# Performance work log

Hardware: AMD Instinct MI355X
Metric: run time of the kernel (lower is better)

The kernel has to match this reference:

```python
import jax, jax.numpy as jnp
import numpy as np

NUM_TYPES = 4
IN_DIM = 128
HID_DIM = 256
OUT_DIM = 128
NUM_NODES = 100000


def setup_inputs() -> dict:
    key = jax.random.key(0)
    k_x, k_t, k_w1, k_b1, k_w2, k_b2 = jax.random.split(key, 6)
    raw_features = jax.random.normal(k_x, (NUM_NODES, IN_DIM), dtype=jnp.float32)
    node_type = jax.random.randint(k_t, (NUM_NODES,), 0, NUM_TYPES, dtype=jnp.int64)
    # stacked per-type MLP params (Kaiming-ish scale like torch Linear defaults)
    W1 = jax.random.uniform(k_w1, (NUM_TYPES, IN_DIM, HID_DIM), dtype=jnp.float32,
                            minval=-1.0, maxval=1.0) / np.sqrt(IN_DIM)
    b1 = jax.random.uniform(k_b1, (NUM_TYPES, HID_DIM), dtype=jnp.float32,
                            minval=-1.0, maxval=1.0) / np.sqrt(IN_DIM)
    W2 = jax.random.uniform(k_w2, (NUM_TYPES, HID_DIM, OUT_DIM), dtype=jnp.float32,
                            minval=-1.0, maxval=1.0) / np.sqrt(HID_DIM)
    b2 = jax.random.uniform(k_b2, (NUM_TYPES, OUT_DIM), dtype=jnp.float32,
                            minval=-1.0, maxval=1.0) / np.sqrt(HID_DIM)
    return {"raw_features": raw_features, "node_type": node_type,
            "W1": W1, "b1": b1, "W2": W2, "b2": b2}


def reference(raw_features, node_type, W1, b1, W2, b2):
    # Run every expert on every node (num_types is tiny), then select per node.
    # h: [types, nodes, hidden]
    h = jax.nn.relu(jnp.einsum('ni,tih->tnh', raw_features, W1) + b1[:, None, :])
    # out_all: [types, nodes, out]
    out_all = jnp.einsum('tnh,tho->tno', h, W2) + b2[:, None, :]
    # select expert output matching each node's type -> [nodes, out]
    encoded = out_all[node_type, jnp.arange(raw_features.shape[0])]
    return encoded
```

## Files before the change

kernel.cpp:

```cpp
#include <hip/hip_runtime.h>
#include <hip/hip_bf16.h>

typedef float f32x4 __attribute__((ext_vector_type(4)));
typedef short short8 __attribute__((ext_vector_type(8)));

#define NTYPES 4


static __device__ __forceinline__ unsigned short f2bf(float f) {
  union { float f; unsigned int u; } v; v.f = f;
  unsigned int u = v.u;
  unsigned int r = u + 0x7FFFu + ((u >> 16) & 1u);
  return (unsigned short)(r >> 16);
}

static __device__ __forceinline__ unsigned int pkbf(float a, float b) {
  __hip_bfloat162 h = __float22bfloat162_rn(make_float2(a, b));
  union { __hip_bfloat162 h; unsigned int u; } v; v.h = h;
  return v.u;
}

__global__ __launch_bounds__(256) void k_prep(const float* __restrict__ W1,
                                              const float* __restrict__ W2,
                                              unsigned short* __restrict__ W1T,
                                              unsigned short* __restrict__ W2T,
                                              int* __restrict__ meta) {
  __shared__ unsigned short s[64][72];
  const int tid = threadIdx.x;
  const int b = blockIdx.x;
  if (b == 0 && tid < 16) meta[tid] = 0;
  const int bb = b & 31;
  const int t = bb >> 3, ti = bb & 7;
  const float* src; unsigned short* dst; int scols, tr, tc;
  if (b < 32) { src = W1 + t * 32768; dst = W1T + t * 32768; scols = 256; tr = ti >> 2; tc = ti & 3; }
  else        { src = W2 + t * 32768; dst = W2T + t * 32768; scols = 128; tr = ti >> 1; tc = ti & 1; }
  const int srows = 32768 / scols;
  const int r0 = tid >> 4, c4 = (tid & 15) << 2;
  #pragma unroll
  for (int i = 0; i < 4; ++i) {
    int r = tr * 64 + i * 16 + r0;
    float4 v = *(const float4*)(src + r * scols + tc * 64 + c4);
    s[i * 16 + r0][c4 + 0] = f2bf(v.x);
    s[i * 16 + r0][c4 + 1] = f2bf(v.y);
    s[i * 16 + r0][c4 + 2] = f2bf(v.z);
    s[i * 16 + r0][c4 + 3] = f2bf(v.w);
  }
  __syncthreads();
  #pragma unroll
  for (int i = 0; i < 4; ++i) {
    int orow = i * 16 + r0;
    ushort4 u;
    u.x = s[c4 + 0][orow];
    u.y = s[c4 + 1][orow];
    u.z = s[c4 + 2][orow];
    u.w = s[c4 + 3][orow];
    *(ushort4*)(dst + (tc * 64 + orow) * srows + tr * 64 + c4) = u;
  }
}

__global__ __launch_bounds__(256) void k_hist(const int* __restrict__ NT, int n,
                                              int* __restrict__ meta) {
  __shared__ int c[NTYPES];
  if (threadIdx.x < NTYPES) c[threadIdx.x] = 0;
  __syncthreads();
  int i = blockIdx.x * 256 + threadIdx.x;
  if (i < n) atomicAdd(&c[NT[i]], 1);
  __syncthreads();
  if (threadIdx.x < NTYPES && c[threadIdx.x] > 0)
    atomicAdd(&meta[threadIdx.x], c[threadIdx.x]);
}

__global__ __launch_bounds__(256) void k_scatter(const int* __restrict__ NT, int n,
                                                 int* __restrict__ meta,
                                                 int* __restrict__ perm) {
  __shared__ int cnt[NTYPES];
  __shared__ int cbase[NTYPES];
  __shared__ int sb[NTYPES + 1];
  if (threadIdx.x < NTYPES) cnt[threadIdx.x] = 0;
  if (threadIdx.x == 0) {
    int b = 0; sb[0] = 0;
    for (int t = 0; t < NTYPES; ++t) {
      b += (meta[t] + 63) & ~63;
      sb[t + 1] = b;
    }
  }
  __syncthreads();
  int i = blockIdx.x * 256 + threadIdx.x;
  int t = 0, r = 0;
  bool valid = (i < n);
  if (valid) { t = NT[i]; r = atomicAdd(&cnt[t], 1); }
  __syncthreads();
  if (threadIdx.x < NTYPES)
    cbase[threadIdx.x] = atomicAdd(&meta[4 + threadIdx.x], cnt[threadIdx.x]);
  __syncthreads();
  if (valid) perm[sb[t] + cbase[t] + r] = i;
  if (blockIdx.x == 0) {
    if (threadIdx.x <= NTYPES) meta[8 + threadIdx.x] = sb[threadIdx.x];
    int tt = threadIdx.x >> 6, j = threadIdx.x & 63;
    int p = sb[tt] + meta[tt] + j;
    if (p < sb[tt + 1]) perm[p] = -1;
  }
}

__global__ __launch_bounds__(256, 1) void k_mlpw(
    const float* __restrict__ X, const int* __restrict__ perm,
    const int* __restrict__ meta,
    const unsigned short* __restrict__ W1T, const unsigned short* __restrict__ W2T,
    const float* __restrict__ B1, const float* __restrict__ B2,
    float* __restrict__ OUT, float* __restrict__ dump) {
  __shared__ __align__(16) unsigned char x_lds[16384];
  __shared__ __align__(16) unsigned char h_lds[32768];
  __shared__ int s_rid[2][64];

  const int tid = threadIdx.x;
  const int l  = tid & 63, w = tid >> 6;
  const int lo = l & 15,  hi = l >> 4;
  const int rg = tid >> 5;
  const int c4 = (tid & 31) * 4;

  const int t  = blockIdx.x >> 7;
  const int lb = blockIdx.x & 127;
  const int g0 = meta[8 + t] >> 6;
  const int g1 = meta[9 + t] >> 6;
  const int nt = g1 - g0 - lb;
  if (nt <= 0) return;
  const int cnt = (nt + 127) >> 7;

  if (tid < 64) s_rid[0][tid] = perm[(g0 + lb) * 64 + tid];
  __syncthreads();
  float4 xv[8];
  #pragma unroll
  for (int p = 0; p < 8; ++p) {
    int row = p * 8 + rg;
    int rd = s_rid[0][row];
    xv[p] = make_float4(0.f, 0.f, 0.f, 0.f);
    if (rd >= 0) xv[p] = *(const float4*)(X + (size_t)rd * 128 + c4);
  }

  const unsigned short* w1t = W1T + (t << 15);
  const unsigned short* w2t = W2T + (t << 15);
  short8 a1[4][4];
  #pragma unroll
  for (int ks = 0; ks < 4; ++ks)
    #pragma unroll
    for (int m = 0; m < 4; ++m)
      a1[ks][m] = *(const short8*)(w1t + (w * 64 + m * 16 + lo) * 128 + ks * 32 + hi * 8);
  short8 a2[8][2];
  #pragma unroll
  for (int ks = 0; ks < 8; ++ks)
    #pragma unroll
    for (int mo = 0; mo < 2; ++mo)
      a2[ks][mo] = *(const short8*)(w2t + (w * 32 + mo * 16 + lo) * 256 + ks * 32 + hi * 8);
  f32x4 bb1[4], bb2[2];
  #pragma unroll
  for (int m = 0; m < 4; ++m)
    bb1[m] = *(const f32x4*)(B1 + t * 256 + w * 64 + m * 16 + hi * 4);
  #pragma unroll
  for (int mo = 0; mo < 2; ++mo)
    bb2[mo] = *(const f32x4*)(B2 + t * 128 + w * 32 + mo * 16 + hi * 4);

  for (int j = 0; j < cnt; ++j) {
    const int g = g0 + lb + j * 128;
    const bool hn = (j + 1 < cnt);
    const int cur = j & 1, nxt = cur ^ 1;

    #pragma unroll
    for (int p = 0; p < 8; ++p) {
      int row = p * 8 + rg;
      uint2 u;
      u.x = pkbf(xv[p].x, xv[p].y);
      u.y = pkbf(xv[p].z, xv[p].w);
      int byte = (row * 256 + c4 * 2) ^ ((row & 7) << 4);
      *(uint2*)(x_lds + byte) = u;
    }
    __syncthreads();

    if (hn && tid < 64) s_rid[nxt][tid] = perm[(g + 128) * 64 + tid];

    f32x4 acc[4][4];
    #pragma unroll
    for (int m = 0; m < 4; ++m)
      #pragma unroll
      for (int n = 0; n < 4; ++n) acc[m][n] = (f32x4){0.f, 0.f, 0.f, 0.f};
    #pragma unroll
    for (int ks = 0; ks < 4; ++ks) {
      short8 b[4];
      #pragma unroll
      for (int n = 0; n < 4; ++n) {
        int row = n * 16 + lo;
        int byte = (row * 256 + ks * 64 + hi * 16) ^ ((row & 7) << 4);
        b[n] = *(const short8*)(x_lds + byte);
      }
      #pragma unroll
      for (int m = 0; m < 4; ++m)
        #pragma unroll
        for (int n = 0; n < 4; ++n)
          acc[m][n] = __builtin_amdgcn_mfma_f32_16x16x32_bf16(a1[ks][m], b[n], acc[m][n], 0, 0, 0);
    }

    #pragma unroll
    for (int m = 0; m < 4; ++m) {
      const int hw2 = w * 128 + m * 32 + hi * 8;
      #pragma unroll
      for (int n = 0; n < 4; ++n) {
        int node = n * 16 + lo;
        uint2 hu;
        hu.x = pkbf(fmaxf(acc[m][n][0] + bb1[m][0], 0.f),
                    fmaxf(acc[m][n][1] + bb1[m][1], 0.f));
        hu.y = pkbf(fmaxf(acc[m][n][2] + bb1[m][2], 0.f),
                    fmaxf(acc[m][n][3] + bb1[m][3], 0.f));
        int byte = (node * 512 + hw2) ^ ((node & 7) << 4);
        *(uint2*)(h_lds + byte) = hu;
      }
    }
    __syncthreads();

    float4 nv[8];
    #pragma unroll
    for (int p = 0; p < 8; ++p) nv[p] = make_float4(0.f, 0.f, 0.f, 0.f);
    if (hn) {
      #pragma unroll
      for (int p = 0; p < 8; ++p) {
        int rd = s_rid[nxt][p * 8 + rg];
        if (rd >= 0) nv[p] = *(const float4*)(X + (size_t)rd * 128 + c4);
      }
    }

    f32x4 acc2[2][4];
    #pragma unroll
    for (int mo = 0; mo < 2; ++mo)
      #pragma unroll
      for (int n = 0; n < 4; ++n) acc2[mo][n] = (f32x4){0.f, 0.f, 0.f, 0.f};
    #pragma unroll
    for (int ks = 0; ks < 8; ++ks) {
      short8 b[4];
      #pragma unroll
      for (int n = 0; n < 4; ++n) {
        int node = n * 16 + lo;
        int byte = (node * 512 + ks * 64 + hi * 16) ^ ((node & 7) << 4);
        b[n] = *(const short8*)(h_lds + byte);
      }
      #pragma unroll
      for (int mo = 0; mo < 2; ++mo)
        #pragma unroll
        for (int n = 0; n < 4; ++n)
          acc2[mo][n] = __builtin_amdgcn_mfma_f32_16x16x32_bf16(a2[ks][mo], b[n], acc2[mo][n], 0, 0, 0);
    }
    __syncthreads();

    #pragma unroll
    for (int mo = 0; mo < 2; ++mo) {
      const int oc = w * 32 + mo * 16 + hi * 4;
      #pragma unroll
      for (int n = 0; n < 4; ++n) {
        int node = n * 16 + lo;
        f32x4 o = acc2[mo][n];
        o[0] += bb2[mo][0]; o[1] += bb2[mo][1];
        o[2] += bb2[mo][2]; o[3] += bb2[mo][3];
        int byte = (node * 512 + oc * 4) ^ ((node & 7) << 4);
        *(f32x4*)(h_lds + byte) = o;
      }
    }
    __syncthreads();

    #pragma unroll
    for (int p = 0; p < 8; ++p) {
      int row = p * 8 + rg;
      int rd = s_rid[cur][row];
      f32x4 v = *(const f32x4*)(h_lds + ((row * 512 + c4 * 4) ^ ((row & 7) << 4)));
      float* dst = (rd >= 0) ? (OUT + (size_t)rd * 128 + c4) : (dump + c4);
      *(f32x4*)dst = v;
    }

    #pragma unroll
    for (int p = 0; p < 8; ++p) xv[p] = nv[p];
  }
}

extern "C" void kernel_launch(void* const* d_in, const int* in_sizes, int n_in,
                              void* d_out, int out_size, void* d_ws, size_t ws_size,
                              hipStream_t stream) {
  const float* X  = (const float*)d_in[0];
  const int*   NT = (const int*)d_in[1];
  const float* W1 = (const float*)d_in[2];
  const float* B1 = (const float*)d_in[3];
  const float* W2 = (const float*)d_in[4];
  const float* B2 = (const float*)d_in[5];
  float* OUT = (float*)d_out;
  const int n = in_sizes[1];

  char* ws = (char*)d_ws;
  int* meta = (int*)ws;
  float* dump = (float*)(ws + 512);
  int* perm = (int*)(ws + 1024);
  unsigned short* W1T = (unsigned short*)(ws + 402432);
  unsigned short* W2T = (unsigned short*)(ws + 664576);

  k_prep<<<64, 256, 0, stream>>>(W1, W2, W1T, W2T, meta);
  const int nb = (n + 255) / 256;
  k_hist<<<nb, 256, 0, stream>>>(NT, n, meta);
  k_scatter<<<nb, 256, 0, stream>>>(NT, n, meta, perm);
  k_mlpw<<<512, 256, 0, stream>>>(X, perm, meta, W1T, W2T, B1, B2, OUT, dump);
}
```

Baseline: 58.45 us.

## Fuse prep, histogram, scatter and MLP into one cooperative kernel

Replaces the four-kernel pipeline (weight transpose, histogram, scatter, grouped MLP) with a single cooperative kernel of 256 blocks that uses grid-wide syncs between phases. The histogram becomes per-block counts with a deterministic prefix sum instead of global atomics, which also removes the meta zeroing dependency. This removes three kernel launch gaps. In exchange the MLP phase runs with only 256 blocks (64 per type) rather than 512, and two grid barriers are added. A three-kernel fallback path runs if the cooperative launch fails.

```diff
diff --git a/kernel.cpp b/kernel.cpp
--- a/kernel.cpp
+++ b/kernel.cpp
@@ -1,10 +1,14 @@
 #include <hip/hip_runtime.h>
 #include <hip/hip_bf16.h>
+#include <hip/hip_cooperative_groups.h>
+
+namespace cg = cooperative_groups;
 
 typedef float f32x4 __attribute__((ext_vector_type(4)));
 typedef short short8 __attribute__((ext_vector_type(8)));
 
 #define NTYPES 4
+#define GRIDC 256
 
 
 static __device__ __forceinline__ unsigned short f2bf(float f) {
@@ -20,119 +24,61 @@
   return v.u;
 }
 
-__global__ __launch_bounds__(256) void k_prep(const float* __restrict__ W1,
-                                              const float* __restrict__ W2,
-                                              unsigned short* __restrict__ W1T,
-                                              unsigned short* __restrict__ W2T,
-                                              int* __restrict__ meta) {
-  __shared__ unsigned short s[64][72];
-  const int tid = threadIdx.x;
-  const int b = blockIdx.x;
-  if (b == 0 && tid < 16) meta[tid] = 0;
-  const int bb = b & 31;
-  const int t = bb >> 3, ti = bb & 7;
+static __device__ __forceinline__ void prep_tile(int role, int tid,
+    const float* __restrict__ W1, const float* __restrict__ W2,
+    unsigned short* __restrict__ W1T, unsigned short* __restrict__ W2T,
+    unsigned short (*sp)[72]) {
+  const int bb = role & 31;
+  const int tt = bb >> 3, ti = bb & 7;
   const float* src; unsigned short* dst; int scols, tr, tc;
-  if (b < 32) { src = W1 + t * 32768; dst = W1T + t * 32768; scols = 256; tr = ti >> 2; tc = ti & 3; }
-  else        { src = W2 + t * 32768; dst = W2T + t * 32768; scols = 128; tr = ti >> 1; tc = ti & 1; }
+  if (role < 32) { src = W1 + tt * 32768; dst = W1T + tt * 32768; scols = 256; tr = ti >> 2; tc = ti & 3; }
+  else           { src = W2 + tt * 32768; dst = W2T + tt * 32768; scols = 128; tr = ti >> 1; tc = ti & 1; }
   const int srows = 32768 / scols;
-  const int r0 = tid >> 4, c4 = (tid & 15) << 2;
+  const int r0 = tid >> 4, cw = (tid & 15) << 2;
   #pragma unroll
   for (int i = 0; i < 4; ++i) {
     int r = tr * 64 + i * 16 + r0;
-    float4 v = *(const float4*)(src + r * scols + tc * 64 + c4);
-    s[i * 16 + r0][c4 + 0] = f2bf(v.x);
-    s[i * 16 + r0][c4 + 1] = f2bf(v.y);
-    s[i * 16 + r0][c4 + 2] = f2bf(v.z);
-    s[i * 16 + r0][c4 + 3] = f2bf(v.w);
+    float4 v = *(const float4*)(src + r * scols + tc * 64 + cw);
+    sp[i * 16 + r0][cw + 0] = f2bf(v.x);
+    sp[i * 16 + r0][cw + 1] = f2bf(v.y);
+    sp[i * 16 + r0][cw + 2] = f2bf(v.z);
+    sp[i * 16 + r0][cw + 3] = f2bf(v.w);
   }
   __syncthreads();
   #pragma unroll
   for (int i = 0; i < 4; ++i) {
     int orow = i * 16 + r0;
     ushort4 u;
-    u.x = s[c4 + 0][orow];
-    u.y = s[c4 + 1][orow];
-    u.z = s[c4 + 2][orow];
-    u.w = s[c4 + 3][orow];
-    *(ushort4*)(dst + (tc * 64 + orow) * srows + tr * 64 + c4) = u;
-  }
-}
-
-__global__ __launch_bounds__(256) void k_hist(const int* __restrict__ NT, int n,
-                                              int* __restrict__ meta) {
-  __shared__ int c[NTYPES];
-  if (threadIdx.x < NTYPES) c[threadIdx.x] = 0;
-  __syncthreads();
-  int i = blockIdx.x * 256 + threadIdx.x;
-  if (i < n) atomicAdd(&c[NT[i]], 1);
-  __syncthreads();
-  if (threadIdx.x < NTYPES && c[threadIdx.x] > 0)
-    atomicAdd(&meta[threadIdx.x], c[threadIdx.x]);
-}
-
-__global__ __launch_bounds__(256) void k_scatter(const int* __restrict__ NT, int n,
-                                                 int* __restrict__ meta,
-                                                 int* __restrict__ perm) {
-  __shared__ int cnt[NTYPES];
-  __shared__ int cbase[NTYPES];
-  __shared__ int sb[NTYPES + 1];
-  if (threadIdx.x < NTYPES) cnt[threadIdx.x] = 0;
-  if (threadIdx.x == 0) {
-    int b = 0; sb[0] = 0;
-    for (int t = 0; t < NTYPES; ++t) {
-      b += (meta[t] + 63) & ~63;
-      sb[t + 1] = b;
-    }
-  }
-  __syncthreads();
-  int i = blockIdx.x * 256 + threadIdx.x;
-  int t = 0, r = 0;
-  bool valid = (i < n);
-  if (valid) { t = NT[i]; r = atomicAdd(&cnt[t], 1); }
-  __syncthreads();
-  if (threadIdx.x < NTYPES)
-    cbase[threadIdx.x] = atomicAdd(&meta[4 + threadIdx.x], cnt[threadIdx.x]);
-  __syncthreads();
-  if (valid) perm[sb[t] + cbase[t] + r] = i;
-  if (blockIdx.x == 0) {
-    if (threadIdx.x <= NTYPES) meta[8 + threadIdx.x] = sb[threadIdx.x];
-    int tt = threadIdx.x >> 6, j = threadIdx.x & 63;
-    int p = sb[tt] + meta[tt] + j;
-    if (p < sb[tt + 1]) perm[p] = -1;
-  }
-}
-
-__global__ __launch_bounds__(256, 1) void k_mlpw(
+    u.x = sp[cw + 0][orow];
+    u.y = sp[cw + 1][orow];
+    u.z = sp[cw + 2][orow];
+    u.w = sp[cw + 3][orow];
+    *(ushort4*)(dst + (tc * 64 + orow) * srows + tr * 64 + cw) = u;
+  }
+}
+
+static __device__ __forceinline__ void mlp_body(
+    int t, int lb, int nblk, int g0, int g1, int tid,
     const float* __restrict__ X, const int* __restrict__ perm,
-    const int* __restrict__ meta,
     const unsigned short* __restrict__ W1T, const unsigned short* __restrict__ W2T,
     const float* __restrict__ B1, const float* __restrict__ B2,
-    float* __restrict__ OUT, float* __restrict__ dump) {
-  __shared__ __align__(16) unsigned char x_lds[16384];
-  __shared__ __align__(16) unsigned char h_lds[32768];
-  __shared__ int s_rid[2][64];
-
-  const int tid = threadIdx.x;
+    float* __restrict__ OUT, float* __restrict__ dump,
+    unsigned char* x_lds, unsigned char* h_lds, int (*s_rid)[64]) {
   const int l  = tid & 63, w = tid >> 6;
   const int lo = l & 15,  hi = l >> 4;
+  const int nt2 = g1 - g0 - lb;
+  if (nt2 <= 0) return;
+  const int cnt = (nt2 + nblk - 1) / nblk;
+
   const int rg = tid >> 5;
   const int c4 = (tid & 31) * 4;
 
-  const int t  = blockIdx.x >> 7;
-  const int lb = blockIdx.x & 127;
-  const int g0 = meta[8 + t] >> 6;
-  const int g1 = meta[9 + t] >> 6;
-  const int nt = g1 - g0 - lb;
-  if (nt <= 0) return;
-  const int cnt = (nt + 127) >> 7;
-
   if (tid < 64) s_rid[0][tid] = perm[(g0 + lb) * 64 + tid];
   __syncthreads();
   float4 xv[8];
   #pragma unroll
   for (int p = 0; p < 8; ++p) {
-    int row = p * 8 + rg;
-    int rd = s_rid[0][row];
+    int rd = s_rid[0][p * 8 + rg];
     xv[p] = make_float4(0.f, 0.f, 0.f, 0.f);
     if (rd >= 0) xv[p] = *(const float4*)(X + (size_t)rd * 128 + c4);
   }
@@ -160,7 +106,7 @@
     bb2[mo] = *(const f32x4*)(B2 + t * 128 + w * 32 + mo * 16 + hi * 4);
 
   for (int j = 0; j < cnt; ++j) {
-    const int g = g0 + lb + j * 128;
+    const int g = g0 + lb + j * nblk;
     const bool hn = (j + 1 < cnt);
     const int cur = j & 1, nxt = cur ^ 1;
 
@@ -175,40 +121,40 @@
     }
     __syncthreads();
 
-    if (hn && tid < 64) s_rid[nxt][tid] = perm[(g + 128) * 64 + tid];
+    if (hn && tid < 64) s_rid[nxt][tid] = perm[(g + nblk) * 64 + tid];
 
     f32x4 acc[4][4];
     #pragma unroll
     for (int m = 0; m < 4; ++m)
       #pragma unroll
-      for (int n = 0; n < 4; ++n) acc[m][n] = (f32x4){0.f, 0.f, 0.f, 0.f};
+      for (int n2 = 0; n2 < 4; ++n2) acc[m][n2] = (f32x4){0.f, 0.f, 0.f, 0.f};
     #pragma unroll
     for (int ks = 0; ks < 4; ++ks) {
       short8 b[4];
       #pragma unroll
-      for (int n = 0; n < 4; ++n) {
-        int row = n * 16 + lo;
+      for (int n2 = 0; n2 < 4; ++n2) {
+        int row = n2 * 16 + lo;
         int byte = (row * 256 + ks * 64 + hi * 16) ^ ((row & 7) << 4);
-        b[n] = *(const short8*)(x_lds + byte);
+        b[n2] = *(const short8*)(x_lds + byte);
       }
       #pragma unroll
       for (int m = 0; m < 4; ++m)
         #pragma unroll
-        for (int n = 0; n < 4; ++n)
-          acc[m][n] = __builtin_amdgcn_mfma_f32_16x16x32_bf16(a1[ks][m], b[n], acc[m][n], 0, 0, 0);
+        for (int n2 = 0; n2 < 4; ++n2)
+          acc[m][n2] = __builtin_amdgcn_mfma_f32_16x16x32_bf16(a1[ks][m], b[n2], acc[m][n2], 0, 0, 0);
     }
 
     #pragma unroll
     for (int m = 0; m < 4; ++m) {
       const int hw2 = w * 128 + m * 32 + hi * 8;
       #pragma unroll
-      for (int n = 0; n < 4; ++n) {
-        int node = n * 16 + lo;
+      for (int n2 = 0; n2 < 4; ++n2) {
+        int node = n2 * 16 + lo;
         uint2 hu;
-        hu.x = pkbf(fmaxf(acc[m][n][0] + bb1[m][0], 0.f),
-                    fmaxf(acc[m][n][1] + bb1[m][1], 0.f));
-        hu.y = pkbf(fmaxf(acc[m][n][2] + bb1[m][2], 0.f),
-                    fmaxf(acc[m][n][3] + bb1[m][3], 0.f));
+        hu.x = pkbf(fmaxf(acc[m][n2][0] + bb1[m][0], 0.f),
+                    fmaxf(acc[m][n2][1] + bb1[m][1], 0.f));
+        hu.y = pkbf(fmaxf(acc[m][n2][2] + bb1[m][2], 0.f),
+                    fmaxf(acc[m][n2][3] + bb1[m][3], 0.f));
         int byte = (node * 512 + hw2) ^ ((node & 7) << 4);
         *(uint2*)(h_lds + byte) = hu;
       }
@@ -230,21 +176,21 @@
     #pragma unroll
     for (int mo = 0; mo < 2; ++mo)
       #pragma unroll
-      for (int n = 0; n < 4; ++n) acc2[mo][n] = (f32x4){0.f, 0.f, 0.f, 0.f};
+      for (int n2 = 0; n2 < 4; ++n2) acc2[mo][n2] = (f32x4){0.f, 0.f, 0.f, 0.f};
     #pragma unroll
     for (int ks = 0; ks < 8; ++ks) {
       short8 b[4];
       #pragma unroll
-      for (int n = 0; n < 4; ++n) {
-        int node = n * 16 + lo;
+      for (int n2 = 0; n2 < 4; ++n2) {
+        int node = n2 * 16 + lo;
         int byte = (node * 512 + ks * 64 + hi * 16) ^ ((node & 7) << 4);
-        b[n] = *(const short8*)(h_lds + byte);
+        b[n2] = *(const short8*)(h_lds + byte);
       }
       #pragma unroll
       for (int mo = 0; mo < 2; ++mo)
         #pragma unroll
-        for (int n = 0; n < 4; ++n)
-          acc2[mo][n] = __builtin_amdgcn_mfma_f32_16x16x32_bf16(a2[ks][mo], b[n], acc2[mo][n], 0, 0, 0);
+        for (int n2 = 0; n2 < 4; ++n2)
+          acc2[mo][n2] = __builtin_amdgcn_mfma_f32_16x16x32_bf16(a2[ks][mo], b[n2], acc2[mo][n2], 0, 0, 0);
     }
     __syncthreads();
 
@@ -252,9 +198,9 @@
     for (int mo = 0; mo < 2; ++mo) {
       const int oc = w * 32 + mo * 16 + hi * 4;
       #pragma unroll
-      for (int n = 0; n < 4; ++n) {
-        int node = n * 16 + lo;
-        f32x4 o = acc2[mo][n];
+      for (int n2 = 0; n2 < 4; ++n2) {
+        int node = n2 * 16 + lo;
+        f32x4 o = acc2[mo][n2];
         o[0] += bb2[mo][0]; o[1] += bb2[mo][1];
         o[2] += bb2[mo][2]; o[3] += bb2[mo][3];
         int byte = (node * 512 + oc * 4) ^ ((node & 7) << 4);
@@ -275,6 +221,157 @@
     #pragma unroll
     for (int p = 0; p < 8; ++p) xv[p] = nv[p];
   }
+}
+
+__global__ __launch_bounds__(256, 1) void k_all(
+    const float* __restrict__ X, const int* __restrict__ NT,
+    const float* __restrict__ W1, const float* __restrict__ B1,
+    const float* __restrict__ W2, const float* __restrict__ B2,
+    float* __restrict__ OUT, int n,
+    int* __restrict__ perm, int* __restrict__ cnts,
+    unsigned short* __restrict__ W1T, unsigned short* __restrict__ W2T,
+    float* __restrict__ dump) {
+  __shared__ __align__(16) unsigned char x_lds[16384];
+  __shared__ __align__(16) unsigned char h_lds[32768];
+  __shared__ int s_rid[2][64];
+  __shared__ int lcnt[NTYPES];
+  __shared__ int s_tot[NTYPES], s_pre[NTYPES];
+
+  const int tid = threadIdx.x;
+  const int bid = blockIdx.x;
+  const int l = tid & 63, w = tid >> 6;
+
+  const int span = (n + GRIDC - 1) / GRIDC;
+  const int sA = bid * span;
+  const int sB = min(n, sA + span);
+  if (tid < NTYPES) lcnt[tid] = 0;
+  __syncthreads();
+  for (int i = sA + tid; i < sB; i += 256) atomicAdd(&lcnt[NT[i]], 1);
+  __syncthreads();
+  if (tid < NTYPES) cnts[bid * NTYPES + tid] = lcnt[tid];
+
+  if (bid < 64)
+    prep_tile(bid, tid, W1, W2, W1T, W2T, (unsigned short (*)[72])h_lds);
+
+  cg::this_grid().sync();
+
+  {
+    int tot = 0, pre = 0;
+    #pragma unroll
+    for (int q = 0; q < 4; ++q) {
+      int b = l * 4 + q;
+      int c = cnts[b * NTYPES + w];
+      tot += c;
+      pre += (b < bid) ? c : 0;
+    }
+    #pragma unroll
+    for (int off = 32; off; off >>= 1) {
+      tot += __shfl_down(tot, off);
+      pre += __shfl_down(pre, off);
+    }
+    if (l == 0) { s_tot[w] = tot; s_pre[w] = pre; }
+  }
+  __syncthreads();
+  int sb[NTYPES + 1];
+  sb[0] = 0;
+  #pragma unroll
+  for (int tau = 0; tau < NTYPES; ++tau)
+    sb[tau + 1] = sb[tau] + ((s_tot[tau] + 63) & ~63);
+
+  if (tid < NTYPES) lcnt[tid] = 0;
+  __syncthreads();
+  for (int i = sA + tid; i < sB; i += 256) {
+    int tt = NT[i];
+    int r = atomicAdd(&lcnt[tt], 1);
+    perm[sb[tt] + s_pre[tt] + r] = i;
+  }
+  if ((bid & 63) == 0) {
+    int tau = bid >> 6;
+    for (int p = sb[tau] + s_tot[tau] + tid; p < sb[tau + 1]; p += 256)
+      perm[p] = -1;
+  }
+
+  cg::this_grid().sync();
+
+  const int t = bid >> 6, lb = bid & 63;
+  mlp_body(t, lb, 64, sb[t] >> 6, sb[t + 1] >> 6, tid,
+           X, perm, W1T, W2T, B1, B2, OUT, dump, x_lds, h_lds, s_rid);
+}
+
+__global__ __launch_bounds__(256) void k_hp(
+    const float* __restrict__ W1, const float* __restrict__ W2,
+    unsigned short* __restrict__ W1T, unsigned short* __restrict__ W2T,
+    const int* __restrict__ NT, int n, int* __restrict__ cnts) {
+  __shared__ unsigned short sp[64][72];
+  __shared__ int lc[NTYPES];
+  const int tid = threadIdx.x;
+  if (blockIdx.x < 64) {
+    prep_tile(blockIdx.x, tid, W1, W2, W1T, W2T, sp);
+  } else {
+    int hb = blockIdx.x - 64;
+    if (tid < NTYPES) lc[tid] = 0;
+    __syncthreads();
+    int i = hb * 256 + tid;
+    if (i < n) atomicAdd(&lc[NT[i]], 1);
+    __syncthreads();
+    if (tid < NTYPES) cnts[hb * NTYPES + tid] = lc[tid];
+  }
+}
+
+__global__ __launch_bounds__(256) void k_scatter2(
+    const int* __restrict__ NT, int n, const int* __restrict__ cnts, int nbH,
+    int* __restrict__ perm, int* __restrict__ bases) {
+  __shared__ int s_tot[NTYPES], s_pre[NTYPES], lc[NTYPES];
+  const int tid = threadIdx.x;
+  const int bid = blockIdx.x;
+  const int l = tid & 63, w = tid >> 6;
+  {
+    int tot = 0, pre = 0;
+    for (int b = l; b < nbH; b += 64) {
+      int c = cnts[b * NTYPES + w];
+      tot += c;
+      pre += (b < bid) ? c : 0;
+    }
+    #pragma unroll
+    for (int off = 32; off; off >>= 1) {
+      tot += __shfl_down(tot, off);
+      pre += __shfl_down(pre, off);
+    }
+    if (l == 0) { s_tot[w] = tot; s_pre[w] = pre; }
+  }
+  __syncthreads();
+  int sb[NTYPES + 1];
+  sb[0] = 0;
+  #pragma unroll
+  for (int tau = 0; tau < NTYPES; ++tau)
+    sb[tau + 1] = sb[tau] + ((s_tot[tau] + 63) & ~63);
+  if (bid == 0 && tid <= NTYPES) bases[tid] = sb[tid];
+  if (tid < NTYPES) lc[tid] = 0;
+  __syncthreads();
+  int i = bid * 256 + tid;
+  if (i < n) {
+    int tt = NT[i];
+    int r = atomicAdd(&lc[tt], 1);
+    perm[sb[tt] + s_pre[tt] + r] = i;
+  }
+  if (bid < NTYPES) {
+    for (int p = sb[bid] + s_tot[bid] + tid; p < sb[bid + 1]; p += 256)
+      perm[p] = -1;
+  }
+}
+
+__global__ __launch_bounds__(256, 1) void k_mlpw_fb(
+    const float* __restrict__ X, const int* __restrict__ perm,
+    const int* __restrict__ bases,
+    const unsigned short* __restrict__ W1T, const unsigned short* __restrict__ W2T,
+    const float* __restrict__ B1, const float* __restrict__ B2,
+    float* __restrict__ OUT, float* __restrict__ dump) {
+  __shared__ __align__(16) unsigned char x_lds[16384];
+  __shared__ __align__(16) unsigned char h_lds[32768];
+  __shared__ int s_rid[2][64];
+  const int t = blockIdx.x >> 7, lb = blockIdx.x & 127;
+  mlp_body(t, lb, 128, bases[t] >> 6, bases[t + 1] >> 6, threadIdx.x,
+           X, perm, W1T, W2T, B1, B2, OUT, dump, x_lds, h_lds, s_rid);
 }
 
 extern "C" void kernel_launch(void* const* d_in, const int* in_sizes, int n_in,
@@ -287,18 +384,32 @@
   const float* W2 = (const float*)d_in[4];
   const float* B2 = (const float*)d_in[5];
   float* OUT = (float*)d_out;
-  const int n = in_sizes[1];
+  int n = in_sizes[1];
 
   char* ws = (char*)d_ws;
-  int* meta = (int*)ws;
   float* dump = (float*)(ws + 512);
-  int* perm = (int*)(ws + 1024);
-  unsigned short* W1T = (unsigned short*)(ws + 402432);
-  unsigned short* W2T = (unsigned short*)(ws + 664576);
-
-  k_prep<<<64, 256, 0, stream>>>(W1, W2, W1T, W2T, meta);
-  const int nb = (n + 255) / 256;
-  k_hist<<<nb, 256, 0, stream>>>(NT, n, meta);
-  k_scatter<<<nb, 256, 0, stream>>>(NT, n, meta, perm);
-  k_mlpw<<<512, 256, 0, stream>>>(X, perm, meta, W1T, W2T, B1, B2, OUT, dump);
-}
+  int* bases = (int*)(ws + 2048);
+  int* cnts = (int*)(ws + 4096);
+  int* perm = (int*)(ws + 16384);
+  unsigned short* W1T = (unsigned short*)(ws + 524288);
+  unsigned short* W2T = (unsigned short*)(ws + 786432);
+
+  void* args[13];
+  args[0]  = (void*)&X;    args[1]  = (void*)&NT;
+  args[2]  = (void*)&W1;   args[3]  = (void*)&B1;
+  args[4]  = (void*)&W2;   args[5]  = (void*)&B2;
+  args[6]  = (void*)&OUT;  args[7]  = (void*)&n;
+  args[8]  = (void*)&perm; args[9]  = (void*)&cnts;
+  args[10] = (void*)&W1T;  args[11] = (void*)&W2T;
+  args[12] = (void*)&dump;
+
+  hipError_t e = hipLaunchCooperativeKernel((const void*)k_all, dim3(GRIDC),
+                                            dim3(256), args, 0, stream);
+  if (e != hipSuccess) {
+    (void)hipGetLastError();
+    const int nbH = (n + 255) / 256;
+    k_hp<<<64 + nbH, 256, 0, stream>>>(W1, W2, W1T, W2T, NT, n, cnts);
+    k_scatter2<<<nbH, 256, 0, stream>>>(NT, n, cnts, nbH, perm, bases);
+    k_mlpw_fb<<<512, 256, 0, stream>>>(X, perm, bases, W1T, W2T, B1, B2, OUT, dump);
+  }
+}
```

After: 110.2 us. 1.88x slower.
